# Kernel optimization log

Measured on AMD Instinct MI355X. Metric: run time of the kernel, lower is better.

Reference implementation:

```python
import jax, jax.numpy as jnp
import numpy as np

GROUP_SIZE = 64
SCALING = 1.0  # lora_alpha / r = 16 / 16
# bitsandbytes NF4 codebook (16 normal-float levels)
NF4_CODE = jnp.array([
    -1.0, -0.6961928009986877, -0.5250730514526367, -0.39491748809814453,
    -0.28444138169288635, -0.18477343022823334, -0.09105003625154495, 0.0,
    0.07958029955625534, 0.16093020141124725, 0.24611230194568634,
    0.33791524171829224, 0.44070982933044434, 0.5626170039176941,
    0.7229568362236023, 1.0], dtype=jnp.float32)

IN_F, OUT_F, R, TOKENS = 4096, 11008, 16, 32


def setup_inputs() -> dict:
    key = jax.random.key(0)
    k0, k1, k2, k3, k4 = jax.random.split(key, 5)
    x = jax.random.normal(k0, (TOKENS, IN_F), dtype=jnp.float32)
    # each byte packs two 4-bit NF4 indices (high nibble first)
    packed_weight = jax.random.randint(k1, (OUT_F * IN_F // 2,), 0, 256, dtype=jnp.int32)
    # per-group absmax scales (positive)
    scales = jax.random.uniform(k2, (OUT_F * IN_F // GROUP_SIZE,), dtype=jnp.float32,
                                minval=0.005, maxval=0.05)
    lora_A = jax.random.normal(k3, (R, IN_F), dtype=jnp.float32) * 0.02
    lora_B = jax.random.normal(k4, (OUT_F, R), dtype=jnp.float32) * 0.02
    return {"x": x, "packed_weight": packed_weight, "scales": scales,
            "lora_A": lora_A, "lora_B": lora_B}


def _dequant_nf4(packed_weight, scales):
    hi = packed_weight // 16          # first nibble
    lo = packed_weight % 16           # second nibble
    idx = jnp.stack([hi, lo], axis=-1).reshape(-1)          # [out*in]
    w = NF4_CODE[idx].reshape(-1, GROUP_SIZE) * scales[:, None]
    return w.reshape(OUT_F, IN_F)                            # [out, in]


def reference(x, packed_weight, scales, lora_A, lora_B):
    W = _dequant_nf4(packed_weight, scales)
    base = x @ W.T                                           # [tokens, out]
    lora = (x @ lora_A.T) @ lora_B.T                         # low-rank update
    return base + SCALING * lora
```

## Files before the change

kernel.cpp:

```cpp
#include <hip/hip_runtime.h>
#include <hip/hip_bf16.h>

#define IN_F 4096
#define OUT_F 11008
#define TOKENS 32
#define RANK 16
#define KSPLIT 8
#define KSLICE (IN_F / KSPLIT)
#define XPAD 520
#define OUT_ELEMS (TOKENS * OUT_F)

typedef unsigned short u16;
typedef __attribute__((ext_vector_type(8))) short bf16x8;
typedef __attribute__((ext_vector_type(4))) float f32x4;
typedef __attribute__((ext_vector_type(4))) int i32x4;

__device__ const float NF4_d[16] = {
    -1.0f, -0.6961928009986877f, -0.5250730514526367f, -0.39491748809814453f,
    -0.28444138169288635f, -0.18477343022823334f, -0.09105003625154495f, 0.0f,
    0.07958029955625534f, 0.16093020141124725f, 0.24611230194568634f,
    0.33791524171829224f, 0.44070982933044434f, 0.5626170039176941f,
    0.7229568362236023f, 1.0f};

static __device__ __forceinline__ unsigned pk2(float a, float b) {
    __hip_bfloat162 h = __float22bfloat162_rn(make_float2(a, b));
    unsigned u;
    __builtin_memcpy(&u, &h, 4);
    return u;
}

__global__ void prep_xa_zero(const float* __restrict__ x, const float* __restrict__ A,
                             float* __restrict__ xa, float* __restrict__ out) {
    __shared__ float red[256];
    if (blockIdx.x >= 512) {
        int i = (blockIdx.x - 512) * 256 + threadIdx.x;
        float4 z = make_float4(0.f, 0.f, 0.f, 0.f);
        for (int j = i; j < OUT_ELEMS / 4; j += 16384) ((float4*)out)[j] = z;
        return;
    }
    int b = blockIdx.x;
    int t = b >> 4, r = b & 15;
    const float4* xr = (const float4*)(x + t * IN_F);
    const float4* ar = (const float4*)(A + r * IN_F);
    float s = 0.f;
    for (int c = 0; c < 4; ++c) {
        int j = c * 256 + threadIdx.x;
        float4 xv = xr[j], av = ar[j];
        s += xv.x * av.x + xv.y * av.y + xv.z * av.z + xv.w * av.w;
    }
    red[threadIdx.x] = s;
    __syncthreads();
    for (int st = 128; st > 0; st >>= 1) {
        if (threadIdx.x < st) red[threadIdx.x] += red[threadIdx.x + st];
        __syncthreads();
    }
    if (threadIdx.x == 0) xa[b] = red[0];
}

__global__ __launch_bounds__(256, 4) void qlora_fused(
    const int* __restrict__ packed, const float* __restrict__ scales,
    const float* __restrict__ x, const float* __restrict__ xa,
    const float* __restrict__ B, float* __restrict__ out) {
    __shared__ u16 xs[32 * XPAD];
    __shared__ unsigned tbl[256];
    __shared__ float xal[512];
    const int tid = threadIdx.x;
    const int kbase = blockIdx.y * KSLICE;

    const int lane = tid & 63;
    const int wv = tid >> 6;
    const int n = lane & 15;
    const int q = lane >> 4;
    const int olo = blockIdx.x * 128 + wv * 32 + n;
    const int ohi = olo + 16;

    const i32x4* pp0 = (const i32x4*)(packed + olo * 2048 + (kbase >> 1)) + q;
    const i32x4* pp1 = (const i32x4*)(packed + ohi * 2048 + (kbase >> 1)) + q;
    i32x4 P0[2], P1[2];
    P0[0] = __builtin_nontemporal_load(pp0);
    P1[0] = __builtin_nontemporal_load(pp1);
    P0[1] = __builtin_nontemporal_load(pp0 + 4);
    P1[1] = __builtin_nontemporal_load(pp1 + 4);

    const float4* sp0 = (const float4*)(scales + olo * 64 + (kbase >> 6));
    const float4* sp1 = (const float4*)(scales + ohi * 64 + (kbase >> 6));
    float4 s0A = sp0[0], s0B = sp0[1];
    float4 s1A = sp1[0], s1B = sp1[1];

    tbl[tid] = pk2(NF4_d[tid & 15], NF4_d[tid >> 4]);

    if (blockIdx.y == 0) {
        xal[tid] = xa[tid];
        xal[tid + 256] = xa[tid + 256];
    }

    for (int it = 0; it < 8; ++it) {
        int row = it * 4 + (tid >> 6);
        int c8 = tid & 63;
        const float4* src = (const float4*)(x + row * IN_F + kbase + c8 * 8);
        float4 v0 = src[0], v1 = src[1];
        uint4 d;
        d.x = pk2(v0.x, v0.y);
        d.y = pk2(v0.z, v0.w);
        d.z = pk2(v1.x, v1.y);
        d.w = pk2(v1.z, v1.w);
        *(uint4*)(xs + row * XPAD + c8 * 8) = d;
    }
    __syncthreads();

    f32x4 acc00 = {0.f, 0.f, 0.f, 0.f};
    f32x4 acc10 = {0.f, 0.f, 0.f, 0.f};
    f32x4 acc01 = {0.f, 0.f, 0.f, 0.f};
    f32x4 acc11 = {0.f, 0.f, 0.f, 0.f};
    const u16* xr0 = xs + n * XPAD + q * 8;
    const u16* xr1 = xs + (n + 16) * XPAD + q * 8;
    const float sc0r[8] = {s0A.x, s0A.y, s0A.z, s0A.w, s0B.x, s0B.y, s0B.z, s0B.w};
    const float sc1r[8] = {s1A.x, s1A.y, s1A.z, s1A.w, s1B.x, s1B.y, s1B.z, s1B.w};

#pragma unroll
    for (int s = 0; s < 16; ++s) {
        i32x4 c0 = P0[s & 1];
        i32x4 c1 = P1[s & 1];
        if (s + 2 < 16) {
            P0[s & 1] = __builtin_nontemporal_load(pp0 + (s + 2) * 4);
            P1[s & 1] = __builtin_nontemporal_load(pp1 + (s + 2) * 4);
        }
        float sc0 = sc0r[s >> 1];
        float sc1 = sc1r[s >> 1];

        uint4 b0u, b1u;
        {
            unsigned u0 = tbl[c0[0] & 255], u1 = tbl[c0[1] & 255];
            unsigned u2 = tbl[c0[2] & 255], u3 = tbl[c0[3] & 255];
            b0u.x = pk2(__int_as_float(u0 & 0xFFFF0000u) * sc0, __int_as_float(u0 << 16) * sc0);
            b0u.y = pk2(__int_as_float(u1 & 0xFFFF0000u) * sc0, __int_as_float(u1 << 16) * sc0);
            b0u.z = pk2(__int_as_float(u2 & 0xFFFF0000u) * sc0, __int_as_float(u2 << 16) * sc0);
            b0u.w = pk2(__int_as_float(u3 & 0xFFFF0000u) * sc0, __int_as_float(u3 << 16) * sc0);
        }
        {
            unsigned u0 = tbl[c1[0] & 255], u1 = tbl[c1[1] & 255];
            unsigned u2 = tbl[c1[2] & 255], u3 = tbl[c1[3] & 255];
            b1u.x = pk2(__int_as_float(u0 & 0xFFFF0000u) * sc1, __int_as_float(u0 << 16) * sc1);
            b1u.y = pk2(__int_as_float(u1 & 0xFFFF0000u) * sc1, __int_as_float(u1 << 16) * sc1);
            b1u.z = pk2(__int_as_float(u2 & 0xFFFF0000u) * sc1, __int_as_float(u2 << 16) * sc1);
            b1u.w = pk2(__int_as_float(u3 & 0xFFFF0000u) * sc1, __int_as_float(u3 << 16) * sc1);
        }
        bf16x8 bf0, bf1;
        __builtin_memcpy(&bf0, &b0u, 16);
        __builtin_memcpy(&bf1, &b1u, 16);
        bf16x8 a0 = *(const bf16x8*)(xr0 + s * 32);
        bf16x8 a1 = *(const bf16x8*)(xr1 + s * 32);
        acc00 = __builtin_amdgcn_mfma_f32_16x16x32_bf16(a0, bf0, acc00, 0, 0, 0);
        acc10 = __builtin_amdgcn_mfma_f32_16x16x32_bf16(a1, bf0, acc10, 0, 0, 0);
        acc01 = __builtin_amdgcn_mfma_f32_16x16x32_bf16(a0, bf1, acc01, 0, 0, 0);
        acc11 = __builtin_amdgcn_mfma_f32_16x16x32_bf16(a1, bf1, acc11, 0, 0, 0);
    }

    if (blockIdx.y == 0) {
        const float4* brl = (const float4*)(B + olo * RANK);
        const float4* brh = (const float4*)(B + ohi * RANK);
        float4 l0 = brl[0], l1 = brl[1], l2 = brl[2], l3 = brl[3];
        float4 h0 = brh[0], h1 = brh[1], h2 = brh[2], h3 = brh[3];
#pragma unroll
        for (int r = 0; r < 4; ++r) {
            int t = q * 4 + r;
#pragma unroll
            for (int half = 0; half < 2; ++half) {
                int tt = t + half * 16;
                const float4* xt = (const float4*)(xal + tt * RANK);
                float4 x0 = xt[0], x1 = xt[1], x2 = xt[2], x3 = xt[3];
                float lorL = l0.x * x0.x + l0.y * x0.y + l0.z * x0.z + l0.w * x0.w +
                             l1.x * x1.x + l1.y * x1.y + l1.z * x1.z + l1.w * x1.w +
                             l2.x * x2.x + l2.y * x2.y + l2.z * x2.z + l2.w * x2.w +
                             l3.x * x3.x + l3.y * x3.y + l3.z * x3.z + l3.w * x3.w;
                float lorH = h0.x * x0.x + h0.y * x0.y + h0.z * x0.z + h0.w * x0.w +
                             h1.x * x1.x + h1.y * x1.y + h1.z * x1.z + h1.w * x1.w +
                             h2.x * x2.x + h2.y * x2.y + h2.z * x2.z + h2.w * x2.w +
                             h3.x * x3.x + h3.y * x3.y + h3.z * x3.z + h3.w * x3.w;
                float aL = half ? acc10[r] : acc00[r];
                float aH = half ? acc11[r] : acc01[r];
                atomicAdd(out + tt * OUT_F + olo, aL + lorL);
                atomicAdd(out + tt * OUT_F + ohi, aH + lorH);
            }
        }
    } else {
#pragma unroll
        for (int r = 0; r < 4; ++r) {
            int t = q * 4 + r;
            atomicAdd(out + t * OUT_F + olo, acc00[r]);
            atomicAdd(out + (t + 16) * OUT_F + olo, acc10[r]);
            atomicAdd(out + t * OUT_F + ohi, acc01[r]);
            atomicAdd(out + (t + 16) * OUT_F + ohi, acc11[r]);
        }
    }
}

extern "C" void kernel_launch(void* const* d_in, const int* in_sizes, int n_in,
                              void* d_out, int out_size, void* d_ws, size_t ws_size,
                              hipStream_t stream) {
    const float* x = (const float*)d_in[0];
    const int* packed = (const int*)d_in[1];
    const float* scales = (const float*)d_in[2];
    const float* lora_A = (const float*)d_in[3];
    const float* lora_B = (const float*)d_in[4];
    float* out = (float*)d_out;

    float* xa = (float*)d_ws;

    prep_xa_zero<<<576, 256, 0, stream>>>(x, lora_A, xa, out);
    qlora_fused<<<dim3(OUT_F / 128, KSPLIT), 256, 0, stream>>>(packed, scales, x, xa,
                                                               lora_B, out);
}
```

Measured before the change: 152.8 us.

## Replace atomic split-K accumulation with partial buffers and a fused reduce+LoRA kernel

```diff
diff --git a/kernel.cpp b/kernel.cpp
--- a/kernel.cpp
+++ b/kernel.cpp
@@ -9,6 +9,7 @@
 #define KSLICE (IN_F / KSPLIT)
 #define XPAD 520
 #define OUT_ELEMS (TOKENS * OUT_F)
+#define NGEMM (86 * KSPLIT)
 
 typedef unsigned short u16;
 typedef __attribute__((ext_vector_type(8))) short bf16x8;
@@ -29,49 +30,42 @@
     return u;
 }
 
-__global__ void prep_xa_zero(const float* __restrict__ x, const float* __restrict__ A,
-                             float* __restrict__ xa, float* __restrict__ out) {
-    __shared__ float red[256];
-    if (blockIdx.x >= 512) {
-        int i = (blockIdx.x - 512) * 256 + threadIdx.x;
-        float4 z = make_float4(0.f, 0.f, 0.f, 0.f);
-        for (int j = i; j < OUT_ELEMS / 4; j += 16384) ((float4*)out)[j] = z;
-        return;
-    }
-    int b = blockIdx.x;
-    int t = b >> 4, r = b & 15;
-    const float4* xr = (const float4*)(x + t * IN_F);
-    const float4* ar = (const float4*)(A + r * IN_F);
-    float s = 0.f;
-    for (int c = 0; c < 4; ++c) {
-        int j = c * 256 + threadIdx.x;
-        float4 xv = xr[j], av = ar[j];
-        s += xv.x * av.x + xv.y * av.y + xv.z * av.z + xv.w * av.w;
-    }
-    red[threadIdx.x] = s;
-    __syncthreads();
-    for (int st = 128; st > 0; st >>= 1) {
-        if (threadIdx.x < st) red[threadIdx.x] += red[threadIdx.x + st];
-        __syncthreads();
-    }
-    if (threadIdx.x == 0) xa[b] = red[0];
-}
-
-__global__ __launch_bounds__(256, 4) void qlora_fused(
+__global__ __launch_bounds__(256, 4) void qlora_part_xa(
     const int* __restrict__ packed, const float* __restrict__ scales,
-    const float* __restrict__ x, const float* __restrict__ xa,
-    const float* __restrict__ B, float* __restrict__ out) {
+    const float* __restrict__ x, const float* __restrict__ A,
+    float* __restrict__ part, float* __restrict__ xa) {
     __shared__ u16 xs[32 * XPAD];
     __shared__ unsigned tbl[256];
-    __shared__ float xal[512];
     const int tid = threadIdx.x;
-    const int kbase = blockIdx.y * KSLICE;
+
+    if (blockIdx.x >= NGEMM) {
+        int b = blockIdx.x - NGEMM;
+        int t = b >> 4, r = b & 15;
+        const float4* xr = (const float4*)(x + t * IN_F);
+        const float4* ar = (const float4*)(A + r * IN_F);
+        float s = 0.f;
+        for (int c = 0; c < 4; ++c) {
+            int j = c * 256 + tid;
+            float4 xv = xr[j], av = ar[j];
+            s += xv.x * av.x + xv.y * av.y + xv.z * av.z + xv.w * av.w;
+        }
+        for (int off = 32; off > 0; off >>= 1) s += __shfl_down(s, off, 64);
+        __shared__ float w4[4];
+        if ((tid & 63) == 0) w4[tid >> 6] = s;
+        __syncthreads();
+        if (tid == 0) xa[b] = w4[0] + w4[1] + w4[2] + w4[3];
+        return;
+    }
+
+    const int bx = blockIdx.x % 86;
+    const int by = blockIdx.x / 86;
+    const int kbase = by * KSLICE;
 
     const int lane = tid & 63;
     const int wv = tid >> 6;
     const int n = lane & 15;
     const int q = lane >> 4;
-    const int olo = blockIdx.x * 128 + wv * 32 + n;
+    const int olo = bx * 128 + wv * 32 + n;
     const int ohi = olo + 16;
 
     const i32x4* pp0 = (const i32x4*)(packed + olo * 2048 + (kbase >> 1)) + q;
@@ -88,11 +82,6 @@
     float4 s1A = sp1[0], s1B = sp1[1];
 
     tbl[tid] = pk2(NF4_d[tid & 15], NF4_d[tid >> 4]);
-
-    if (blockIdx.y == 0) {
-        xal[tid] = xa[tid];
-        xal[tid + 256] = xa[tid + 256];
-    }
 
     for (int it = 0; it < 8; ++it) {
         int row = it * 4 + (tid >> 6);
@@ -156,43 +145,54 @@
         acc11 = __builtin_amdgcn_mfma_f32_16x16x32_bf16(a1, bf1, acc11, 0, 0, 0);
     }
 
-    if (blockIdx.y == 0) {
-        const float4* brl = (const float4*)(B + olo * RANK);
-        const float4* brh = (const float4*)(B + ohi * RANK);
-        float4 l0 = brl[0], l1 = brl[1], l2 = brl[2], l3 = brl[3];
-        float4 h0 = brh[0], h1 = brh[1], h2 = brh[2], h3 = brh[3];
-#pragma unroll
-        for (int r = 0; r < 4; ++r) {
-            int t = q * 4 + r;
-#pragma unroll
-            for (int half = 0; half < 2; ++half) {
-                int tt = t + half * 16;
-                const float4* xt = (const float4*)(xal + tt * RANK);
-                float4 x0 = xt[0], x1 = xt[1], x2 = xt[2], x3 = xt[3];
-                float lorL = l0.x * x0.x + l0.y * x0.y + l0.z * x0.z + l0.w * x0.w +
-                             l1.x * x1.x + l1.y * x1.y + l1.z * x1.z + l1.w * x1.w +
-                             l2.x * x2.x + l2.y * x2.y + l2.z * x2.z + l2.w * x2.w +
-                             l3.x * x3.x + l3.y * x3.y + l3.z * x3.z + l3.w * x3.w;
-                float lorH = h0.x * x0.x + h0.y * x0.y + h0.z * x0.z + h0.w * x0.w +
-                             h1.x * x1.x + h1.y * x1.y + h1.z * x1.z + h1.w * x1.w +
-                             h2.x * x2.x + h2.y * x2.y + h2.z * x2.z + h2.w * x2.w +
-                             h3.x * x3.x + h3.y * x3.y + h3.z * x3.z + h3.w * x3.w;
-                float aL = half ? acc10[r] : acc00[r];
-                float aH = half ? acc11[r] : acc01[r];
-                atomicAdd(out + tt * OUT_F + olo, aL + lorL);
-                atomicAdd(out + tt * OUT_F + ohi, aH + lorH);
-            }
-        }
-    } else {
-#pragma unroll
-        for (int r = 0; r < 4; ++r) {
-            int t = q * 4 + r;
-            atomicAdd(out + t * OUT_F + olo, acc00[r]);
-            atomicAdd(out + (t + 16) * OUT_F + olo, acc10[r]);
-            atomicAdd(out + t * OUT_F + ohi, acc01[r]);
-            atomicAdd(out + (t + 16) * OUT_F + ohi, acc11[r]);
-        }
-    }
+    float* pb = part + by * OUT_ELEMS;
+#pragma unroll
+    for (int r = 0; r < 4; ++r) {
+        int t = q * 4 + r;
+        __builtin_nontemporal_store(acc00[r], pb + t * OUT_F + olo);
+        __builtin_nontemporal_store(acc10[r], pb + (t + 16) * OUT_F + olo);
+        __builtin_nontemporal_store(acc01[r], pb + t * OUT_F + ohi);
+        __builtin_nontemporal_store(acc11[r], pb + (t + 16) * OUT_F + ohi);
+    }
+}
+
+__global__ void reduce_lora(const float* __restrict__ part,
+                            const float* __restrict__ xa,
+                            const float* __restrict__ B,
+                            float* __restrict__ out) {
+    int idx4 = blockIdx.x * 256 + threadIdx.x;
+    int t = idx4 / (OUT_F / 4);
+    int o4 = idx4 - t * (OUT_F / 4);
+    int base = t * OUT_F + o4 * 4;
+
+    float4 s = *(const float4*)(part + base);
+#pragma unroll
+    for (int y = 1; y < KSPLIT; ++y) {
+        float4 p = *(const float4*)(part + y * OUT_ELEMS + base);
+        s.x += p.x;
+        s.y += p.y;
+        s.z += p.z;
+        s.w += p.w;
+    }
+
+    const float4* xt = (const float4*)(xa + t * RANK);
+    float4 x0 = xt[0], x1 = xt[1], x2 = xt[2], x3 = xt[3];
+    const float4* br = (const float4*)(B + o4 * 4 * RANK);
+    float res[4];
+#pragma unroll
+    for (int j = 0; j < 4; ++j) {
+        float4 b0 = br[j * 4 + 0], b1 = br[j * 4 + 1];
+        float4 b2 = br[j * 4 + 2], b3 = br[j * 4 + 3];
+        res[j] = b0.x * x0.x + b0.y * x0.y + b0.z * x0.z + b0.w * x0.w +
+                 b1.x * x1.x + b1.y * x1.y + b1.z * x1.z + b1.w * x1.w +
+                 b2.x * x2.x + b2.y * x2.y + b2.z * x2.z + b2.w * x2.w +
+                 b3.x * x3.x + b3.y * x3.y + b3.z * x3.z + b3.w * x3.w;
+    }
+    s.x += res[0];
+    s.y += res[1];
+    s.z += res[2];
+    s.w += res[3];
+    *(float4*)(out + base) = s;
 }
 
 extern "C" void kernel_launch(void* const* d_in, const int* in_sizes, int n_in,
@@ -205,9 +205,9 @@
     const float* lora_B = (const float*)d_in[4];
     float* out = (float*)d_out;
 
-    float* xa = (float*)d_ws;
-
-    prep_xa_zero<<<576, 256, 0, stream>>>(x, lora_A, xa, out);
-    qlora_fused<<<dim3(OUT_F / 128, KSPLIT), 256, 0, stream>>>(packed, scales, x, xa,
-                                                               lora_B, out);
-}
+    float* part = (float*)d_ws;
+    float* xa = (float*)((char*)d_ws + KSPLIT * OUT_ELEMS * 4);
+
+    qlora_part_xa<<<NGEMM + 512, 256, 0, stream>>>(packed, scales, x, lora_A, part, xa);
+    reduce_lora<<<(TOKENS * OUT_F / 4) / 256, 256, 0, stream>>>(part, xa, lora_B, out);
+}
```

Result: slower. 159.1 us (+4.2%).
